# Kernel tuning notes

Measured on AMD Instinct MI355X. Metric: run time of the kernel, lower is better.

## Reference

```python
import jax, jax.numpy as jnp
import numpy as np

T = 5          # temporal frames
WS = 8         # window size (square)
HEADS = 6
DIM = 192      # output channels; qkv input channels = 3*DIM
SHIFT = WS // 2
HDIM = DIM // HEADS
SCALE = HDIM ** -0.5
N = T * WS * WS  # tokens per window = 320


def _rel_index():
    # Faithful replication of the torch buffer construction (including the
    # quirk that the dw channel gets no offset).
    coords = np.stack(np.meshgrid(np.arange(T), np.arange(WS), np.arange(WS), indexing='ij'))
    cf = coords.reshape(3, -1)                      # (3, N)
    rel = (cf[:, :, None] - cf[:, None, :]).transpose(1, 2, 0).astype(np.int64)
    rel[:, :, 0] += WS - 1                          # dt channel
    rel[:, :, 1] += WS - 1                          # dh channel
    rel[:, :, 0] *= 2 * WS - 1
    return rel.sum(-1)                               # (N, N) int

REL_INDEX = jnp.asarray(_rel_index())


def setup_inputs() -> dict:
    key = jax.random.key(0)
    k1, k2, k3, k4 = jax.random.split(key, 4)
    B, H, W = 2, 64, 64
    C = 3 * DIM
    qkv = jax.random.normal(k1, (B, T * H * W, C), jnp.float32)
    bias_table = jax.random.normal(k2, ((T * 2 * WS - 1) * (2 * WS - 1), HEADS), jnp.float32) * 0.02
    proj_w = jax.random.normal(k3, (DIM, DIM), jnp.float32) / np.sqrt(DIM)
    proj_b = jax.random.normal(k4, (DIM,), jnp.float32) * 0.01
    # Standard Swin shifted-window attention mask, tiled over T (t-outer order).
    img = np.zeros((H, W), np.float32)
    cnt = 0
    sls = (slice(0, -WS), slice(-WS, -SHIFT), slice(-SHIFT, None))
    for hs in sls:
        for ws_ in sls:
            img[hs, ws_] = cnt
            cnt += 1
    mw = img.reshape(H // WS, WS, W // WS, WS).transpose(0, 2, 1, 3).reshape(-1, WS * WS)
    mw = np.tile(mw, (1, T))                         # (nW, N)
    am = mw[:, None, :] - mw[:, :, None]
    mask = jnp.asarray(np.where(am != 0, -100.0, 0.0).astype(np.float32))
    return {'qkv': qkv, 'bias_table': bias_table, 'proj_w': proj_w,
            'proj_b': proj_b, 'mask': mask, 'H': H, 'W': W}


def reference(qkv, bias_table, proj_w, proj_b, mask, H, W):
    B, L, C = qkv.shape
    x = qkv.reshape(B, T, H, W, C)
    # cyclic shift
    x = jnp.roll(x, shift=(-SHIFT, -SHIFT), axis=(2, 3))
    # window partition -> (B*nW, N, C)
    x = x.reshape(B, T, H // WS, WS, W // WS, WS, C)
    x = x.transpose(0, 2, 4, 1, 3, 5, 6).reshape(-1, N, C)
    B_ = x.shape[0]
    qkv_ = x.reshape(B_, N, 3, HEADS, HDIM).transpose(2, 0, 3, 1, 4)  # (3,B_,h,N,d)
    q, k, v = qkv_[0] * SCALE, qkv_[1], qkv_[2]
    attn = jnp.einsum('bhqd,bhkd->bhqk', q, k)       # (B_, h, N, N)
    rpb = bias_table[REL_INDEX.reshape(-1)].reshape(N, N, HEADS).transpose(2, 0, 1)
    attn = attn + rpb[None]
    nW = mask.shape[0]
    attn = attn.reshape(B_ // nW, nW, HEADS, N, N) + mask[None, :, None]
    attn = jax.nn.softmax(attn.reshape(B_, HEADS, N, N), axis=-1)
    out = jnp.einsum('bhqk,bhkd->bhqd', attn, v)     # (B_, h, N, d)
    out = out.transpose(0, 2, 1, 3).reshape(B_, N, DIM)
    out = out @ proj_w.T + proj_b
    # window reverse -> (B, T, H, W, DIM)
    out = out.reshape(B, H // WS, W // WS, T, WS, WS, DIM)
    out = out.transpose(0, 3, 1, 4, 2, 5, 6).reshape(B, T, H, W, DIM)
    out = jnp.roll(out, shift=(SHIFT, SHIFT), axis=(2, 3))
    return out.reshape(B, T * H * W, DIM)
```

## Files before the change

### kernel.cpp

```cpp
#include <hip/hip_runtime.h>
#include <hip/hip_bf16.h>

#define TT      5
#define NHEADS  6
#define DIMC    192
#define SHIFT_  4
#define HDIM_   32
#define NTOK    320
#define NWIN    64
#define BATCH   2
#define LOG2E   1.44269504088896f
#define SCALE_LOG2E (0.17677669529663687f * 1.44269504088896f)
#define NEGMASK (-100.0f * 1.44269504088896f)

typedef short short8v __attribute__((ext_vector_type(8)));
typedef float floatx4 __attribute__((ext_vector_type(4)));
union FragU { uint4 u; short8v s; };

static __device__ __forceinline__ float bf16lo(unsigned u) {
    union { unsigned i; float f; } x; x.i = u << 16; return x.f;
}
static __device__ __forceinline__ float bf16hi(unsigned u) {
    union { unsigned i; float f; } x; x.i = u & 0xffff0000u; return x.f;
}
static __device__ __forceinline__ unsigned short bf16b(float f) {
    __hip_bfloat16 h = __float2bfloat16(f);
    unsigned short u; __builtin_memcpy(&u, &h, 2); return u;
}
static __device__ __forceinline__ unsigned pk2(float a, float b) {
    return (unsigned)bf16b(a) | ((unsigned)bf16b(b) << 16);
}
static __device__ __forceinline__ unsigned pk2h(float a, float b) {
    unsigned ua = __float_as_uint(a), ub = __float_as_uint(b);
    return ((ua + 0x8000u) >> 16) | ((ub + 0x8000u) & 0xffff0000u);
}

static __device__ __forceinline__ bool detect_bf16(const unsigned* q) {
    uint4 w = ((const uint4*)q)[threadIdx.x & 63];
    int cnt = 0;
    unsigned e;
    e = (w.x >> 7) & 0xffu; cnt += (e >= 100u && e <= 135u);
    e = (w.y >> 7) & 0xffu; cnt += (e >= 100u && e <= 135u);
    e = (w.z >> 7) & 0xffu; cnt += (e >= 100u && e <= 135u);
    e = (w.w >> 7) & 0xffu; cnt += (e >= 100u && e <= 135u);
    unsigned long long m = __ballot(cnt >= 2);
    return __popcll(m) >= 32;
}

__global__ __launch_bounds__(NTOK) void attn_mfma(
    const void* __restrict__ qkv_raw,
    const void* __restrict__ bias_raw,
    __hip_bfloat16* __restrict__ win_out)
{
    const bool isbf = detect_bf16((const unsigned*)qkv_raw);
    const int b_  = blockIdx.x;
    const int h   = blockIdx.y;
    const int bb  = b_ >> 6;
    const int wdx = b_ & 63;
    const int wi  = wdx >> 3, wj = wdx & 7;
    const int tid = threadIdx.x;
    const int w    = tid >> 6;
    const int lane = tid & 63;
    const int l15  = lane & 15;
    const int quad = lane >> 4;

    __shared__ unsigned short sK[320 * 40];
    __shared__ unsigned short sVT[32 * 328];
    __shared__ float sBias[192];
    __shared__ float sRS[320];

    {
        const int n = tid;
        const int t = n >> 6, s = n & 63, hl = s >> 3, wl = s & 7;
        const int gh = (wi * 8 + hl + SHIFT_) & 63;
        const int gw = (wj * 8 + wl + SHIFT_) & 63;
        const long grow = (long)bb * (TT * 64 * 64) + t * 4096 + gh * 64 + gw;
        const int l32  = n & 31;
        const int slot = (n & ~31) + ((l32 & 4) << 2) + ((l32 >> 3) << 2) + (l32 & 3);
        if (!isbf) {
            const float* base = (const float*)qkv_raw + grow * (3 * DIMC);
            const float* kp = base + DIMC + h * HDIM_;
            uint4* dst = (uint4*)&sK[slot * 40];
            #pragma unroll
            for (int i = 0; i < 4; i++)
                dst[i] = make_uint4(pk2(kp[8*i+0], kp[8*i+1]), pk2(kp[8*i+2], kp[8*i+3]),
                                    pk2(kp[8*i+4], kp[8*i+5]), pk2(kp[8*i+6], kp[8*i+7]));
            const float* vp = base + 2 * DIMC + h * HDIM_;
            #pragma unroll
            for (int d = 0; d < 32; d++) sVT[d * 328 + n] = bf16b(vp[d]);
            if (tid < 192)
                sBias[tid] = ((const float*)bias_raw)[tid * NHEADS + h] * LOG2E;
        } else {
            const __hip_bfloat16* base = (const __hip_bfloat16*)qkv_raw + grow * (3 * DIMC);
            const uint4* kp = (const uint4*)(base + DIMC + h * HDIM_);
            uint4* dst = (uint4*)&sK[slot * 40];
            #pragma unroll
            for (int i = 0; i < 4; i++) dst[i] = kp[i];
            const unsigned* vp = (const unsigned*)(base + 2 * DIMC + h * HDIM_);
            #pragma unroll
            for (int i = 0; i < 16; i++) {
                unsigned u = vp[i];
                sVT[(2*i+0) * 328 + n] = (unsigned short)(u & 0xffffu);
                sVT[(2*i+1) * 328 + n] = (unsigned short)(u >> 16);
            }
            if (tid < 192)
                sBias[tid] = __bfloat162float(((const __hip_bfloat16*)bias_raw)[tid * NHEADS + h]) * LOG2E;
        }
    }

    FragU qf[4];
    int cn_q[4], labq[4];
    #pragma unroll
    for (int jq = 0; jq < 4; jq++) {
        const int qtok = w * 64 + jq * 16 + l15;
        const int t = qtok >> 6, s = qtok & 63, hl = s >> 3, wl = s & 7;
        cn_q[jq] = t * 15 + hl + wl;
        const int hh = wi * 8 + hl, ww = wj * 8 + wl;
        labq[jq] = ((hh < 56) ? 0 : ((hh < 60) ? 1 : 2)) * 3 +
                   ((ww < 56) ? 0 : ((ww < 60) ? 1 : 2));
        const int gh = (wi * 8 + hl + SHIFT_) & 63;
        const int gw = (wj * 8 + wl + SHIFT_) & 63;
        const long grow = (long)bb * (TT * 64 * 64) + t * 4096 + gh * 64 + gw;
        if (!isbf) {
            const float* qp = (const float*)qkv_raw + grow * (3 * DIMC) + h * HDIM_ + quad * 8;
            qf[jq].u = make_uint4(
                pk2(qp[0]*SCALE_LOG2E, qp[1]*SCALE_LOG2E), pk2(qp[2]*SCALE_LOG2E, qp[3]*SCALE_LOG2E),
                pk2(qp[4]*SCALE_LOG2E, qp[5]*SCALE_LOG2E), pk2(qp[6]*SCALE_LOG2E, qp[7]*SCALE_LOG2E));
        } else {
            const uint4 uu = *(const uint4*)((const __hip_bfloat16*)qkv_raw + grow * (3 * DIMC) + h * HDIM_ + quad * 8);
            qf[jq].u = make_uint4(
                pk2(bf16lo(uu.x)*SCALE_LOG2E, bf16hi(uu.x)*SCALE_LOG2E),
                pk2(bf16lo(uu.y)*SCALE_LOG2E, bf16hi(uu.y)*SCALE_LOG2E),
                pk2(bf16lo(uu.z)*SCALE_LOG2E, bf16hi(uu.z)*SCALE_LOG2E),
                pk2(bf16lo(uu.w)*SCALE_LOG2E, bf16hi(uu.w)*SCALE_LOG2E));
        }
    }
    __syncthreads();

    const floatx4 z4 = {0.f, 0.f, 0.f, 0.f};
    floatx4 oacc[4][2];
    #pragma unroll
    for (int i = 0; i < 4; i++) { oacc[i][0] = z4; oacc[i][1] = z4; }
    float rs[4] = {0.f, 0.f, 0.f, 0.f};

    for (int kb = 0; kb < 10; kb++) {
        FragU kf0, kf1, vf0, vf1;
        kf0.u = *(const uint4*)&sK[(kb * 32 + l15) * 40 + quad * 8];
        kf1.u = *(const uint4*)&sK[(kb * 32 + 16 + l15) * 40 + quad * 8];
        vf0.u = *(const uint4*)&sVT[l15 * 328 + kb * 32 + quad * 8];
        vf1.u = *(const uint4*)&sVT[(16 + l15) * 328 + kb * 32 + quad * 8];

        floatx4 sv0[4], sv1[4];
        #pragma unroll
        for (int jq = 0; jq < 4; jq++)
            sv0[jq] = __builtin_amdgcn_mfma_f32_16x16x32_bf16(kf0.s, qf[jq].s, z4, 0, 0, 0);
        #pragma unroll
        for (int jq = 0; jq < 4; jq++)
            sv1[jq] = __builtin_amdgcn_mfma_f32_16x16x32_bf16(kf1.s, qf[jq].s, z4, 0, 0, 0);

        const int Ck   = (7 - (kb >> 1)) * 15 + 7;
        const int sh   = (kb & 1) * 4 + quad;
        const int rhk  = (wi == 7) ? ((sh < 4) ? 1 : 2) : 0;
        const int lab0 = rhk * 3 + ((wj == 7) ? 1 : 0);
        const int lab1 = rhk * 3 + ((wj == 7) ? 2 : 0);
        const int cb   = Ck - sh;

        #pragma unroll
        for (int jq = 0; jq < 4; jq++) {
            const int bidx = cn_q[jq] + cb;
            const float m0 = (lab0 != labq[jq]) ? NEGMASK : 0.f;
            const float m1 = (lab1 != labq[jq]) ? NEGMASK : 0.f;
            float e0[4], e1[4];
            #pragma unroll
            for (int reg = 0; reg < 4; reg++)
                e0[reg] = exp2f(sv0[jq][reg] + sBias[bidx - reg] + m0);
            #pragma unroll
            for (int reg = 0; reg < 4; reg++)
                e1[reg] = exp2f(sv1[jq][reg] + sBias[bidx - 4 - reg] + m1);
            rs[jq] += ((e0[0] + e0[1]) + (e0[2] + e0[3]))
                    + ((e1[0] + e1[1]) + (e1[2] + e1[3]));
            FragU pf;
            pf.u.x = pk2h(e0[0], e0[1]); pf.u.y = pk2h(e0[2], e0[3]);
            pf.u.z = pk2h(e1[0], e1[1]); pf.u.w = pk2h(e1[2], e1[3]);
            oacc[jq][0] = __builtin_amdgcn_mfma_f32_16x16x32_bf16(pf.s, vf0.s, oacc[jq][0], 0, 0, 0);
            oacc[jq][1] = __builtin_amdgcn_mfma_f32_16x16x32_bf16(pf.s, vf1.s, oacc[jq][1], 0, 0, 0);
        }
    }

    #pragma unroll
    for (int jq = 0; jq < 4; jq++) {
        float r = rs[jq];
        r += __shfl_xor(r, 16);
        r += __shfl_xor(r, 32);
        if (lane < 16) sRS[w * 64 + jq * 16 + lane] = r;
    }
    #pragma unroll
    for (int i = 0; i < 4; i++) {
        float inv[4];
        #pragma unroll
        for (int reg = 0; reg < 4; reg++)
            inv[reg] = 1.0f / sRS[w * 64 + i * 16 + quad * 4 + reg];
        #pragma unroll
        for (int nt = 0; nt < 2; nt++) {
            #pragma unroll
            for (int reg = 0; reg < 4; reg++) {
                const int q = w * 64 + i * 16 + quad * 4 + reg;
                win_out[((long)b_ * NTOK + q) * DIMC + h * HDIM_ + nt * 16 + l15] =
                    __float2bfloat16(oacc[i][nt][reg] * inv[reg]);
            }
        }
    }
}

__global__ __launch_bounds__(256) void prep_w(
    const void* __restrict__ w_raw, const void* __restrict__ b_raw,
    const unsigned* __restrict__ sniff,
    unsigned short* __restrict__ wbf, float* __restrict__ bf32)
{
    const bool isbf = detect_bf16(sniff);
    const int g = blockIdx.x * 256 + threadIdx.x;
    if (!isbf) wbf[g] = bf16b(((const float*)w_raw)[g]);
    else       wbf[g] = ((const unsigned short*)w_raw)[g];
    if (blockIdx.x == 0 && threadIdx.x < 192) {
        bf32[threadIdx.x] = isbf
            ? __bfloat162float(((const __hip_bfloat16*)b_raw)[threadIdx.x])
            : ((const float*)b_raw)[threadIdx.x];
    }
}

__global__ __launch_bounds__(256) void proj_mfma(
    const __hip_bfloat16* __restrict__ win,
    const unsigned short* __restrict__ wbf,
    const float* __restrict__ bf32,
    const unsigned* __restrict__ sniff,
    void* __restrict__ out_raw)
{
    const bool isbf = detect_bf16(sniff);
    const int tid  = threadIdx.x;
    const int w    = tid >> 6;
    const int lane = tid & 63;
    const int l15  = lane & 15;
    const int quad = lane >> 4;
    const int tok0 = blockIdx.x * 64 + w * 16;

    const floatx4 z4 = {0.f, 0.f, 0.f, 0.f};
    floatx4 acc[12];
    #pragma unroll
    for (int nt = 0; nt < 12; nt++) acc[nt] = z4;

    #pragma unroll
    for (int ks = 0; ks < 6; ks++) {
        FragU af;
        af.u = *(const uint4*)(win + ((long)tok0 + l15) * DIMC + ks * 32 + quad * 8);
        #pragma unroll
        for (int nt = 0; nt < 12; nt++) {
            FragU bf_;
            bf_.u = *(const uint4*)(wbf + (nt * 16 + l15) * DIMC + ks * 32 + quad * 8);
            acc[nt] = __builtin_amdgcn_mfma_f32_16x16x32_bf16(af.s, bf_.s, acc[nt], 0, 0, 0);
        }
    }

    long rowoff[4];
    #pragma unroll
    for (int reg = 0; reg < 4; reg++) {
        const int token = tok0 + quad * 4 + reg;
        const int bw = token / NTOK;
        const int nn = token - bw * NTOK;
        const int bb = bw >> 6, wdx = bw & 63, wi2 = wdx >> 3, wj2 = wdx & 7;
        const int t = nn >> 6, s2 = nn & 63, hl = s2 >> 3, wl = s2 & 7;
        const int gh = (wi2 * 8 + hl + SHIFT_) & 63;
        const int gw = (wj2 * 8 + wl + SHIFT_) & 63;
        rowoff[reg] = ((long)bb * (TT * 64 * 64) + t * 4096 + gh * 64 + gw) * DIMC;
    }
    #pragma unroll
    for (int nt = 0; nt < 12; nt++) {
        const int o = nt * 16 + l15;
        const float bias = bf32[o];
        #pragma unroll
        for (int reg = 0; reg < 4; reg++) {
            const float v = acc[nt][reg] + bias;
            if (!isbf) ((float*)out_raw)[rowoff[reg] + o] = v;
            else       ((__hip_bfloat16*)out_raw)[rowoff[reg] + o] = __float2bfloat16(v);
        }
    }
}

extern "C" void kernel_launch(void* const* d_in, const int* in_sizes, int n_in,
                              void* d_out, int out_size, void* d_ws, size_t ws_size,
                              hipStream_t stream)
{
    (void)in_sizes; (void)n_in; (void)out_size; (void)ws_size;
    const void* qkv        = d_in[0];
    const void* bias_table = d_in[1];
    const void* proj_w     = d_in[2];
    const void* proj_b     = d_in[3];

    __hip_bfloat16* win = (__hip_bfloat16*)d_ws;
    unsigned short* wbf = (unsigned short*)((char*)d_ws + 15728640);
    float*          bfb = (float*)((char*)d_ws + 15802368);

    prep_w<<<dim3(144), 256, 0, stream>>>(proj_w, proj_b, (const unsigned*)qkv, wbf, bfb);
    attn_mfma<<<dim3(BATCH * NWIN, NHEADS), NTOK, 0, stream>>>(qkv, bias_table, win);
    proj_mfma<<<dim3(BATCH * NWIN * NTOK / 64), 256, 0, stream>>>(
        win, wbf, bfb, (const unsigned*)qkv, d_out);
}
```

Before: 238.3 us.

## Coalesce K/V staging loads and transpose MFMA outputs for vectorized stores

K/V staging now has 8 lanes share each token row and issue float4/uint2 loads, where before each thread loaded a whole token row with scalar loads. This makes the strided global gathers coalesce better. In the PV and projection MFMAs the operand order is swapped so the accumulator holds 4 consecutive channels per lane. That lets the output and projection results be written as packed uint2/float4 stores, and removes the shared-memory row-sum round trip. The risks are bank conflicts on the sVT transposed writes and any layout mistake in the swapped fragments.

Measured after the change: 249.0 us. +4.5%, slower.

```diff
diff --git a/kernel.cpp b/kernel.cpp
--- a/kernel.cpp
+++ b/kernel.cpp
@@ -63,48 +63,75 @@
     const int lane = tid & 63;
     const int l15  = lane & 15;
     const int quad = lane >> 4;
+    const int g    = lane >> 3;
+    const int li   = lane & 7;
 
     __shared__ unsigned short sK[320 * 40];
     __shared__ unsigned short sVT[32 * 328];
     __shared__ float sBias[192];
-    __shared__ float sRS[320];
+
+    if (tid < 192)
+        sBias[tid] = (isbf ? __bfloat162float(((const __hip_bfloat16*)bias_raw)[tid * NHEADS + h])
+                           : ((const float*)bias_raw)[tid * NHEADS + h]) * LOG2E;
 
     {
-        const int n = tid;
-        const int t = n >> 6, s = n & 63, hl = s >> 3, wl = s & 7;
-        const int gh = (wi * 8 + hl + SHIFT_) & 63;
-        const int gw = (wj * 8 + wl + SHIFT_) & 63;
-        const long grow = (long)bb * (TT * 64 * 64) + t * 4096 + gh * 64 + gw;
-        const int l32  = n & 31;
-        const int slot = (n & ~31) + ((l32 & 4) << 2) + ((l32 >> 3) << 2) + (l32 & 3);
+        const int btok = w * 64;
         if (!isbf) {
-            const float* base = (const float*)qkv_raw + grow * (3 * DIMC);
-            const float* kp = base + DIMC + h * HDIM_;
-            uint4* dst = (uint4*)&sK[slot * 40];
-            #pragma unroll
-            for (int i = 0; i < 4; i++)
-                dst[i] = make_uint4(pk2(kp[8*i+0], kp[8*i+1]), pk2(kp[8*i+2], kp[8*i+3]),
-                                    pk2(kp[8*i+4], kp[8*i+5]), pk2(kp[8*i+6], kp[8*i+7]));
-            const float* vp = base + 2 * DIMC + h * HDIM_;
-            #pragma unroll
-            for (int d = 0; d < 32; d++) sVT[d * 328 + n] = bf16b(vp[d]);
-            if (tid < 192)
-                sBias[tid] = ((const float*)bias_raw)[tid * NHEADS + h] * LOG2E;
+            const float* q32 = (const float*)qkv_raw;
+            #pragma unroll
+            for (int r = 0; r < 8; r++) {
+                const int token = btok + r * 8 + g;
+                const int t = token >> 6, s = token & 63;
+                const int gh = (wi * 8 + (s >> 3) + SHIFT_) & 63;
+                const int gw = (wj * 8 + (s & 7) + SHIFT_) & 63;
+                const long grow = (long)bb * (TT * 64 * 64) + t * 4096 + gh * 64 + gw;
+                const float4 kv = *(const float4*)(q32 + grow * (3 * DIMC) + DIMC + h * HDIM_ + li * 4);
+                const int l32 = token & 31;
+                const int slot = (token & ~31) + ((l32 & 4) << 2) + ((l32 >> 3) << 2) + (l32 & 3);
+                *(uint2*)&sK[slot * 40 + li * 4] = make_uint2(pk2(kv.x, kv.y), pk2(kv.z, kv.w));
+            }
+            #pragma unroll
+            for (int r = 0; r < 8; r++) {
+                const int token = btok + r * 8 + g;
+                const int t = token >> 6, s = token & 63;
+                const int gh = (wi * 8 + (s >> 3) + SHIFT_) & 63;
+                const int gw = (wj * 8 + (s & 7) + SHIFT_) & 63;
+                const long grow = (long)bb * (TT * 64 * 64) + t * 4096 + gh * 64 + gw;
+                const float4 vv = *(const float4*)(q32 + grow * (3 * DIMC) + 2 * DIMC + h * HDIM_ + li * 4);
+                const int d0 = li * 4;
+                sVT[(d0 + 0) * 328 + token] = bf16b(vv.x);
+                sVT[(d0 + 1) * 328 + token] = bf16b(vv.y);
+                sVT[(d0 + 2) * 328 + token] = bf16b(vv.z);
+                sVT[(d0 + 3) * 328 + token] = bf16b(vv.w);
+            }
         } else {
-            const __hip_bfloat16* base = (const __hip_bfloat16*)qkv_raw + grow * (3 * DIMC);
-            const uint4* kp = (const uint4*)(base + DIMC + h * HDIM_);
-            uint4* dst = (uint4*)&sK[slot * 40];
-            #pragma unroll
-            for (int i = 0; i < 4; i++) dst[i] = kp[i];
-            const unsigned* vp = (const unsigned*)(base + 2 * DIMC + h * HDIM_);
-            #pragma unroll
-            for (int i = 0; i < 16; i++) {
-                unsigned u = vp[i];
-                sVT[(2*i+0) * 328 + n] = (unsigned short)(u & 0xffffu);
-                sVT[(2*i+1) * 328 + n] = (unsigned short)(u >> 16);
+            const unsigned short* q16 = (const unsigned short*)qkv_raw;
+            #pragma unroll
+            for (int r = 0; r < 8; r++) {
+                const int token = btok + r * 8 + g;
+                const int t = token >> 6, s = token & 63;
+                const int gh = (wi * 8 + (s >> 3) + SHIFT_) & 63;
+                const int gw = (wj * 8 + (s & 7) + SHIFT_) & 63;
+                const long grow = (long)bb * (TT * 64 * 64) + t * 4096 + gh * 64 + gw;
+                const uint2 kv = *(const uint2*)(q16 + grow * (3 * DIMC) + DIMC + h * HDIM_ + li * 4);
+                const int l32 = token & 31;
+                const int slot = (token & ~31) + ((l32 & 4) << 2) + ((l32 >> 3) << 2) + (l32 & 3);
+                *(uint2*)&sK[slot * 40 + li * 4] = kv;
             }
-            if (tid < 192)
-                sBias[tid] = __bfloat162float(((const __hip_bfloat16*)bias_raw)[tid * NHEADS + h]) * LOG2E;
+            #pragma unroll
+            for (int r = 0; r < 8; r++) {
+                const int token = btok + r * 8 + g;
+                const int t = token >> 6, s = token & 63;
+                const int gh = (wi * 8 + (s >> 3) + SHIFT_) & 63;
+                const int gw = (wj * 8 + (s & 7) + SHIFT_) & 63;
+                const long grow = (long)bb * (TT * 64 * 64) + t * 4096 + gh * 64 + gw;
+                const uint2 vv = *(const uint2*)(q16 + grow * (3 * DIMC) + 2 * DIMC + h * HDIM_ + li * 4);
+                const int d0 = li * 4;
+                sVT[(d0 + 0) * 328 + token] = (unsigned short)(vv.x & 0xffffu);
+                sVT[(d0 + 1) * 328 + token] = (unsigned short)(vv.x >> 16);
+                sVT[(d0 + 2) * 328 + token] = (unsigned short)(vv.y & 0xffffu);
+                sVT[(d0 + 3) * 328 + token] = (unsigned short)(vv.y >> 16);
+            }
         }
     }
 
@@ -182,32 +209,24 @@
             FragU pf;
             pf.u.x = pk2h(e0[0], e0[1]); pf.u.y = pk2h(e0[2], e0[3]);
             pf.u.z = pk2h(e1[0], e1[1]); pf.u.w = pk2h(e1[2], e1[3]);
-            oacc[jq][0] = __builtin_amdgcn_mfma_f32_16x16x32_bf16(pf.s, vf0.s, oacc[jq][0], 0, 0, 0);
-            oacc[jq][1] = __builtin_amdgcn_mfma_f32_16x16x32_bf16(pf.s, vf1.s, oacc[jq][1], 0, 0, 0);
-        }
-    }
-
+            oacc[jq][0] = __builtin_amdgcn_mfma_f32_16x16x32_bf16(vf0.s, pf.s, oacc[jq][0], 0, 0, 0);
+            oacc[jq][1] = __builtin_amdgcn_mfma_f32_16x16x32_bf16(vf1.s, pf.s, oacc[jq][1], 0, 0, 0);
+        }
+    }
+
+    unsigned short* wp = (unsigned short*)win_out;
     #pragma unroll
     for (int jq = 0; jq < 4; jq++) {
         float r = rs[jq];
         r += __shfl_xor(r, 16);
         r += __shfl_xor(r, 32);
-        if (lane < 16) sRS[w * 64 + jq * 16 + lane] = r;
-    }
-    #pragma unroll
-    for (int i = 0; i < 4; i++) {
-        float inv[4];
-        #pragma unroll
-        for (int reg = 0; reg < 4; reg++)
-            inv[reg] = 1.0f / sRS[w * 64 + i * 16 + quad * 4 + reg];
+        const float inv = 1.0f / r;
+        const long ob = ((long)b_ * NTOK + (w * 64 + jq * 16 + l15)) * DIMC + h * HDIM_ + quad * 4;
         #pragma unroll
         for (int nt = 0; nt < 2; nt++) {
-            #pragma unroll
-            for (int reg = 0; reg < 4; reg++) {
-                const int q = w * 64 + i * 16 + quad * 4 + reg;
-                win_out[((long)b_ * NTOK + q) * DIMC + h * HDIM_ + nt * 16 + l15] =
-                    __float2bfloat16(oacc[i][nt][reg] * inv[reg]);
-            }
+            const floatx4 o = oacc[jq][nt];
+            *(uint2*)&wp[ob + nt * 16] =
+                make_uint2(pk2(o[0] * inv, o[1] * inv), pk2(o[2] * inv, o[3] * inv));
         }
     }
 }
@@ -250,37 +269,35 @@
 
     #pragma unroll
     for (int ks = 0; ks < 6; ks++) {
-        FragU af;
-        af.u = *(const uint4*)(win + ((long)tok0 + l15) * DIMC + ks * 32 + quad * 8);
+        FragU xf;
+        xf.u = *(const uint4*)((const unsigned short*)win + ((long)tok0 + l15) * DIMC + ks * 32 + quad * 8);
         #pragma unroll
         for (int nt = 0; nt < 12; nt++) {
-            FragU bf_;
-            bf_.u = *(const uint4*)(wbf + (nt * 16 + l15) * DIMC + ks * 32 + quad * 8);
-            acc[nt] = __builtin_amdgcn_mfma_f32_16x16x32_bf16(af.s, bf_.s, acc[nt], 0, 0, 0);
-        }
-    }
-
-    long rowoff[4];
-    #pragma unroll
-    for (int reg = 0; reg < 4; reg++) {
-        const int token = tok0 + quad * 4 + reg;
-        const int bw = token / NTOK;
-        const int nn = token - bw * NTOK;
-        const int bb = bw >> 6, wdx = bw & 63, wi2 = wdx >> 3, wj2 = wdx & 7;
-        const int t = nn >> 6, s2 = nn & 63, hl = s2 >> 3, wl = s2 & 7;
-        const int gh = (wi2 * 8 + hl + SHIFT_) & 63;
-        const int gw = (wj2 * 8 + wl + SHIFT_) & 63;
-        rowoff[reg] = ((long)bb * (TT * 64 * 64) + t * 4096 + gh * 64 + gw) * DIMC;
-    }
+            FragU wf;
+            wf.u = *(const uint4*)(wbf + (nt * 16 + l15) * DIMC + ks * 32 + quad * 8);
+            acc[nt] = __builtin_amdgcn_mfma_f32_16x16x32_bf16(wf.s, xf.s, acc[nt], 0, 0, 0);
+        }
+    }
+
+    const int token = tok0 + l15;
+    const int bw = token / NTOK;
+    const int nn = token - bw * NTOK;
+    const int bb = bw >> 6, wdx = bw & 63, wi2 = wdx >> 3, wj2 = wdx & 7;
+    const int t = nn >> 6, s2 = nn & 63, hl = s2 >> 3, wl = s2 & 7;
+    const int gh = (wi2 * 8 + hl + SHIFT_) & 63;
+    const int gw = (wj2 * 8 + wl + SHIFT_) & 63;
+    const long rowoff = ((long)bb * (TT * 64 * 64) + t * 4096 + gh * 64 + gw) * DIMC;
+
     #pragma unroll
     for (int nt = 0; nt < 12; nt++) {
-        const int o = nt * 16 + l15;
-        const float bias = bf32[o];
-        #pragma unroll
-        for (int reg = 0; reg < 4; reg++) {
-            const float v = acc[nt][reg] + bias;
-            if (!isbf) ((float*)out_raw)[rowoff[reg] + o] = v;
-            else       ((__hip_bfloat16*)out_raw)[rowoff[reg] + o] = __float2bfloat16(v);
+        const float4 bv = *(const float4*)&bf32[nt * 16 + quad * 4];
+        const float o0 = acc[nt][0] + bv.x, o1 = acc[nt][1] + bv.y;
+        const float o2 = acc[nt][2] + bv.z, o3 = acc[nt][3] + bv.w;
+        const long off = rowoff + nt * 16 + quad * 4;
+        if (!isbf) {
+            *(float4*)((float*)out_raw + off) = make_float4(o0, o1, o2, o3);
+        } else {
+            *(uint2*)((unsigned short*)out_raw + off) = make_uint2(pk2(o0, o1), pk2(o2, o3));
         }
     }
 }
```
